# Kernel optimization log

Hardware: AMD Instinct MI355X
Metric: run time of the kernel (lower is better)

## Reference

```python
import jax, jax.numpy as jnp
import numpy as np

N = 100000   # nodes
E = 1600000  # edges (before self-loops)
IN = 128     # in_features
H = 4        # heads
C = 64       # out_features per head
D = H * C    # concat output dim = 256
NEG_SLOPE = 0.2
EPS = 1e-5


def setup_inputs() -> dict:
    key = jax.random.key(0)
    k = jax.random.split(key, 8)
    x = jax.random.normal(k[0], (N, IN), jnp.float32)
    edge_index = jax.random.randint(k[1], (2, E), 0, N, jnp.int32)
    # GATConv params (glorot-ish init)
    W = jax.random.normal(k[2], (IN, D), jnp.float32) * np.float32(np.sqrt(2.0 / (IN + D)))
    att_src = jax.random.normal(k[3], (H, C), jnp.float32) * np.float32(np.sqrt(2.0 / C))
    att_dst = jax.random.normal(k[4], (H, C), jnp.float32) * np.float32(np.sqrt(2.0 / C))
    bias = jnp.zeros((D,), jnp.float32)
    # LayerNorm params
    gamma = jnp.ones((D,), jnp.float32)
    beta = jnp.zeros((D,), jnp.float32)
    return {"x": x, "edge_index": edge_index, "W": W, "att_src": att_src,
            "att_dst": att_dst, "bias": bias, "gamma": gamma, "beta": beta}


def reference(x, edge_index, W, att_src, att_dst, bias, gamma, beta):
    # --- GATConv (add_self_loops=True, negative_slope=0.2, eval-mode dropout) ---
    loops = jnp.arange(N, dtype=edge_index.dtype)
    ei = jnp.concatenate([edge_index, jnp.stack([loops, loops])], axis=1)  # (2, E+N)
    src, dst = ei[0], ei[1]

    h = (x @ W).reshape(N, H, C)                       # (N,H,C)
    a_s = jnp.einsum('nhc,hc->nh', h, att_src)          # (N,H)
    a_d = jnp.einsum('nhc,hc->nh', h, att_dst)          # (N,H)

    logits = jax.nn.leaky_relu(a_s[src] + a_d[dst], NEG_SLOPE)  # (Etot,H)
    # segment softmax over incoming edges of each destination node
    mx = jax.ops.segment_max(logits, dst, num_segments=N)       # (N,H)
    ex = jnp.exp(logits - mx[dst])
    den = jax.ops.segment_sum(ex, dst, num_segments=N)          # (N,H)
    alpha = ex / den[dst]                                       # (Etot,H)

    msg = h[src] * alpha[:, :, None]                             # (Etot,H,C)
    out = jax.ops.segment_sum(msg, dst, num_segments=N)          # (N,H,C)
    out = out.reshape(N, D) + bias

    # --- ELU + LayerNorm (dropout = identity in eval) ---
    out = jax.nn.elu(out)
    mu = out.mean(-1, keepdims=True)
    var = out.var(-1, keepdims=True)
    out = (out - mu) * jax.lax.rsqrt(var + EPS) * gamma + beta
    return out
```

## Files before the change

### kernel.cpp

```cpp
#include <hip/hip_runtime.h>
#include <hip/hip_bf16.h>

#define IN_F 128
#define DF   256
#define HEADS 4
#define CPH  64
#define NEG  0.2f
#define LN_EPS 1e-5f

__device__ __forceinline__ float lrelu(float x) { return x > 0.f ? x : NEG * x; }
__device__ __forceinline__ float b2f(unsigned short u) {
    union { unsigned int i; float f; } v; v.i = ((unsigned int)u) << 16; return v.f;
}

__global__ __launch_bounds__(256) void k_gemm(
        const float* __restrict__ x, const float* __restrict__ W,
        const float* __restrict__ att_s, const float* __restrict__ att_d,
        __hip_bfloat16* __restrict__ hb,
        float* __restrict__ a_s, float* __restrict__ a_d, int N)
{
    __shared__ float xs[16 * IN_F];
    int t = threadIdx.x;
    int row0 = blockIdx.x * 16;

    const float4* xg = (const float4*)(x + (size_t)row0 * IN_F);
    float4* xs4 = (float4*)xs;
    #pragma unroll
    for (int j = 0; j < 2; ++j) {
        int s = t + j * 256;
        if (row0 + (s >> 5) < N) xs4[s] = xg[s];
        else xs4[s] = make_float4(0.f, 0.f, 0.f, 0.f);
    }
    __syncthreads();

    float acc[16];
    #pragma unroll
    for (int r = 0; r < 16; ++r) acc[r] = 0.f;

    const float* Wc = W + t;
    for (int k0 = 0; k0 < IN_F; k0 += 4) {
        float w0 = Wc[(k0 + 0) * DF];
        float w1 = Wc[(k0 + 1) * DF];
        float w2 = Wc[(k0 + 2) * DF];
        float w3 = Wc[(k0 + 3) * DF];
        #pragma unroll
        for (int r = 0; r < 16; ++r) {
            float4 xv = xs4[r * 32 + (k0 >> 2)];
            acc[r] = fmaf(xv.x, w0, fmaf(xv.y, w1, fmaf(xv.z, w2, fmaf(xv.w, w3, acc[r]))));
        }
    }

    int lane = t & 63, wid = t >> 6;
    float was = att_s[t], wad = att_d[t];
    #pragma unroll
    for (int r = 0; r < 16; ++r) {
        int row = row0 + r;
        if (row >= N) break;
        hb[(size_t)row * DF + t] = __float2bfloat16(acc[r]);
        float vs = acc[r] * was, vd = acc[r] * wad;
        #pragma unroll
        for (int m = 32; m >= 1; m >>= 1) {
            vs += __shfl_xor(vs, m, 64);
            vd += __shfl_xor(vd, m, 64);
        }
        if (lane == 0) { a_s[row * 4 + wid] = vs; a_d[row * 4 + wid] = vd; }
    }
}

__global__ void k_count(const int* __restrict__ dste, int E, int* __restrict__ indeg)
{
    for (int e = blockIdx.x * blockDim.x + threadIdx.x; e < E; e += gridDim.x * blockDim.x)
        atomicAdd(&indeg[dste[e]], 1);
}

__global__ __launch_bounds__(256) void k_scanA(const int* __restrict__ indeg, int N, int* __restrict__ part)
{
    int t = threadIdx.x, base = blockIdx.x * 1024;
    int s = 0;
    #pragma unroll
    for (int j = 0; j < 4; ++j) { int i = base + t * 4 + j; if (i < N) s += indeg[i]; }
    #pragma unroll
    for (int m = 32; m >= 1; m >>= 1) s += __shfl_xor(s, m, 64);
    __shared__ int red[4];
    if ((t & 63) == 0) red[t >> 6] = s;
    __syncthreads();
    if (t == 0) part[blockIdx.x] = red[0] + red[1] + red[2] + red[3];
}

__global__ __launch_bounds__(128) void k_scanB(const int* __restrict__ part, int NB, int* __restrict__ bloff)
{
    __shared__ int buf[128];
    int t = threadIdx.x;
    int v = (t < NB) ? part[t] : 0;
    buf[t] = v;
    __syncthreads();
    for (int off = 1; off < 128; off <<= 1) {
        int x2 = (t >= off) ? buf[t - off] : 0;
        __syncthreads();
        buf[t] += x2;
        __syncthreads();
    }
    if (t < NB) bloff[t] = buf[t] - v;
}

__global__ __launch_bounds__(256) void k_scanC(const int* __restrict__ indeg, int N,
        const int* __restrict__ bloff, int* __restrict__ offs, int* __restrict__ cur)
{
    int t = threadIdx.x, bid = blockIdx.x, base = bid * 1024;
    int v[4]; int s = 0;
    #pragma unroll
    for (int j = 0; j < 4; ++j) { int i = base + t * 4 + j; v[j] = (i < N) ? indeg[i] : 0; s += v[j]; }
    __shared__ int lds[256];
    lds[t] = s;
    __syncthreads();
    for (int off = 1; off < 256; off <<= 1) {
        int x2 = (t >= off) ? lds[t - off] : 0;
        __syncthreads();
        lds[t] += x2;
        __syncthreads();
    }
    int run = lds[t] - s + bloff[bid];
    #pragma unroll
    for (int j = 0; j < 4; ++j) {
        int i = base + t * 4 + j;
        if (i < N) { offs[i] = run; cur[i] = run; }
        run += v[j];
    }
    if (bid == (int)gridDim.x - 1 && t == 255) offs[N] = run;
}

__global__ void k_scatter(const int* __restrict__ srce, const int* __restrict__ dste, int E,
                          int* __restrict__ cur, int* __restrict__ srclist)
{
    for (int e = blockIdx.x * blockDim.x + threadIdx.x; e < E; e += gridDim.x * blockDim.x) {
        int d = dste[e];
        int p = atomicAdd(&cur[d], 1);
        srclist[p] = srce[e];
    }
}

__global__ __launch_bounds__(256) void k_gather(
        const __hip_bfloat16* __restrict__ hb,
        const float* __restrict__ a_s, const float* __restrict__ a_d,
        const int* __restrict__ offs, const int* __restrict__ srclist,
        const float* __restrict__ bias, const float* __restrict__ gamma,
        const float* __restrict__ beta, float* __restrict__ out, int N)
{
    int wid = threadIdx.x >> 6, lane = threadIdx.x & 63;
    int n = blockIdx.x * 4 + wid;
    if (n >= N) return;
    int head = lane >> 4;
    int d0 = lane << 2;

    float adh = a_d[(size_t)n * 4 + head];
    int beg = offs[n], end = offs[n + 1];

    float acc0, acc1, acc2, acc3, den;
    {
        float as = a_s[(size_t)n * 4 + head];
        float p = expf(lrelu(as + adh));
        den = p;
        ushort4 hv = *(const ushort4*)(hb + (size_t)n * DF + d0);
        acc0 = p * b2f(hv.x); acc1 = p * b2f(hv.y);
        acc2 = p * b2f(hv.z); acc3 = p * b2f(hv.w);
    }

    int e = beg;
    int s_next = (e < end) ? srclist[e] : 0;
    while (e < end) {
        int s = s_next;
        ++e;
        if (e < end) s_next = srclist[e];
        float as = a_s[(size_t)s * 4 + head];
        ushort4 hv = *(const ushort4*)(hb + (size_t)s * DF + d0);
        float p = expf(lrelu(as + adh));
        den += p;
        acc0 = fmaf(p, b2f(hv.x), acc0); acc1 = fmaf(p, b2f(hv.y), acc1);
        acc2 = fmaf(p, b2f(hv.z), acc2); acc3 = fmaf(p, b2f(hv.w), acc3);
    }

    float inv = 1.f / den;
    float4 bia = *(const float4*)(bias + d0);
    float v0 = fmaf(acc0, inv, bia.x);
    float v1 = fmaf(acc1, inv, bia.y);
    float v2 = fmaf(acc2, inv, bia.z);
    float v3 = fmaf(acc3, inv, bia.w);
    v0 = v0 > 0.f ? v0 : expm1f(v0);
    v1 = v1 > 0.f ? v1 : expm1f(v1);
    v2 = v2 > 0.f ? v2 : expm1f(v2);
    v3 = v3 > 0.f ? v3 : expm1f(v3);

    float s1 = v0 + v1 + v2 + v3;
    float s2 = v0 * v0 + v1 * v1 + v2 * v2 + v3 * v3;
    #pragma unroll
    for (int m = 32; m >= 1; m >>= 1) {
        s1 += __shfl_xor(s1, m, 64);
        s2 += __shfl_xor(s2, m, 64);
    }
    float mu = s1 * (1.f / 256.f);
    float var = s2 * (1.f / 256.f) - mu * mu;
    float rs = rsqrtf(var + LN_EPS);
    float4 g  = *(const float4*)(gamma + d0);
    float4 be = *(const float4*)(beta + d0);
    float4 o;
    o.x = (v0 - mu) * rs * g.x + be.x;
    o.y = (v1 - mu) * rs * g.y + be.y;
    o.z = (v2 - mu) * rs * g.z + be.z;
    o.w = (v3 - mu) * rs * g.w + be.w;
    *(float4*)(out + (size_t)n * DF + d0) = o;
}

extern "C" void kernel_launch(void* const* d_in, const int* in_sizes, int n_in,
                              void* d_out, int out_size, void* d_ws, size_t ws_size,
                              hipStream_t stream)
{
    const float* x     = (const float*)d_in[0];
    const int*   ei    = (const int*)d_in[1];
    const float* W     = (const float*)d_in[2];
    const float* att_s = (const float*)d_in[3];
    const float* att_d = (const float*)d_in[4];
    const float* bias  = (const float*)d_in[5];
    const float* gamma = (const float*)d_in[6];
    const float* beta  = (const float*)d_in[7];
    float* out = (float*)d_out;

    int N = in_sizes[0] / IN_F;
    int E = in_sizes[1] / 2;
    const int* srce = ei;
    const int* dste = ei + E;

    char* wsb = (char*)d_ws;
    size_t off = 0;
    auto alloc = [&](size_t bytes) -> void* {
        void* p = wsb + off;
        off += (bytes + 255) & ~(size_t)255;
        return p;
    };
    __hip_bfloat16* hb = (__hip_bfloat16*)alloc((size_t)N * DF * sizeof(__hip_bfloat16));
    float* a_s   = (float*)alloc((size_t)N * 4 * sizeof(float));
    float* a_d   = (float*)alloc((size_t)N * 4 * sizeof(float));
    int*   indeg = (int*)alloc((size_t)N * sizeof(int));
    int*   offs  = (int*)alloc(((size_t)N + 1) * sizeof(int));
    int*   cur   = (int*)alloc((size_t)N * sizeof(int));
    int*   srclist = (int*)alloc((size_t)E * sizeof(int));
    int NB = (N + 1023) / 1024;
    int* part  = (int*)alloc((size_t)NB * sizeof(int));
    int* bloff = (int*)alloc((size_t)NB * sizeof(int));

    hipMemsetAsync(indeg, 0, (size_t)N * sizeof(int), stream);

    k_gemm<<<(N + 15) / 16, 256, 0, stream>>>(x, W, att_s, att_d, hb, a_s, a_d, N);
    k_count<<<2048, 256, 0, stream>>>(dste, E, indeg);
    k_scanA<<<NB, 256, 0, stream>>>(indeg, N, part);
    k_scanB<<<1, 128, 0, stream>>>(part, NB, bloff);
    k_scanC<<<NB, 256, 0, stream>>>(indeg, N, bloff, offs, cur);
    k_scatter<<<2048, 256, 0, stream>>>(srce, dste, E, cur, srclist);
    k_gather<<<(N + 3) / 4, 256, 0, stream>>>(hb, a_s, a_d, offs, srclist, bias, gamma, beta, out, N);
}
```

Measured before the change: 639.5 us.

## Use bf16 MFMA for node projection GEMM and split attention-score kernel

Replaces the scalar fp32 FMA projection x@W with a bf16 MFMA 16x16x32 kernel. W is pre-packed into the MFMA B-fragment layout by a small pack kernel, and x is converted to bf16 into padded LDS. The per-head attention dot products move into a separate k_att kernel that reads the bf16 h back. This trades an extra pass over h and reduced input precision (x and W in bf16) for much higher GEMM throughput.

New measurement: 527.0 us. -17.6%, faster.

```diff
diff --git a/kernel.cpp b/kernel.cpp
--- a/kernel.cpp
+++ b/kernel.cpp
@@ -3,67 +3,130 @@
 
 #define IN_F 128
 #define DF   256
-#define HEADS 4
-#define CPH  64
 #define NEG  0.2f
 #define LN_EPS 1e-5f
+
+typedef __attribute__((ext_vector_type(8))) short bf16x8;
+typedef __attribute__((ext_vector_type(4))) float f32x4;
 
 __device__ __forceinline__ float lrelu(float x) { return x > 0.f ? x : NEG * x; }
 __device__ __forceinline__ float b2f(unsigned short u) {
     union { unsigned int i; float f; } v; v.i = ((unsigned int)u) << 16; return v.f;
 }
-
+__device__ __forceinline__ unsigned short f2b(float f) {
+    union { float f; unsigned int i; } v; v.f = f;
+    unsigned int r = v.i + 0x7FFFu + ((v.i >> 16) & 1u);
+    return (unsigned short)(r >> 16);
+}
+
+__global__ __launch_bounds__(256) void k_pack(const float* __restrict__ W,
+                                              unsigned short* __restrict__ Wp)
+{
+    int t = blockIdx.x * 256 + threadIdx.x;
+    if (t >= 16 * 4 * 64) return;
+    int lane = t & 63, ks = (t >> 6) & 3, ct = t >> 8;
+    int col = ct * 16 + (lane & 15);
+    int kb  = ks * 32 + (lane >> 4) * 8;
+    unsigned short* dst = Wp + (size_t)t * 8;
+    #pragma unroll
+    for (int j = 0; j < 8; ++j)
+        dst[j] = f2b(W[(size_t)(kb + j) * DF + col]);
+}
+
+#define APAD 136
 __global__ __launch_bounds__(256) void k_gemm(
-        const float* __restrict__ x, const float* __restrict__ W,
+        const float* __restrict__ x, const unsigned short* __restrict__ Wp,
+        unsigned short* __restrict__ hb, int N)
+{
+    __shared__ unsigned short lds_a[64 * APAD];
+    int t = threadIdx.x;
+    int row0 = blockIdx.x * 64;
+
+    const float4* xg = (const float4*)x;
+    #pragma unroll
+    for (int j = 0; j < 8; ++j) {
+        int s = t + j * 256;
+        int r = s >> 5, c4 = s & 31;
+        ushort4 w = make_ushort4(0, 0, 0, 0);
+        if (row0 + r < N) {
+            float4 xv = xg[(size_t)(row0 + r) * 32 + c4];
+            w = make_ushort4(f2b(xv.x), f2b(xv.y), f2b(xv.z), f2b(xv.w));
+        }
+        *(ushort4*)(&lds_a[r * APAD + c4 * 4]) = w;
+    }
+    __syncthreads();
+
+    int lane = t & 63, wid = t >> 6;
+    int rbase = (wid & 1) * 32;
+    int cbase = (wid >> 1) * 128;
+    int ct0 = cbase >> 4;
+
+    bf16x8 af[2][4];
+    #pragma unroll
+    for (int rt = 0; rt < 2; ++rt)
+        #pragma unroll
+        for (int ks = 0; ks < 4; ++ks) {
+            int r = rbase + rt * 16 + (lane & 15);
+            int k = ks * 32 + (lane >> 4) * 8;
+            af[rt][ks] = *(const bf16x8*)(&lds_a[r * APAD + k]);
+        }
+
+    f32x4 acc[2][8];
+    #pragma unroll
+    for (int rt = 0; rt < 2; ++rt)
+        #pragma unroll
+        for (int ct = 0; ct < 8; ++ct)
+            acc[rt][ct] = (f32x4){0.f, 0.f, 0.f, 0.f};
+
+    const bf16x8* Wp8 = (const bf16x8*)Wp;
+    #pragma unroll
+    for (int ct = 0; ct < 8; ++ct) {
+        #pragma unroll
+        for (int ks = 0; ks < 4; ++ks) {
+            bf16x8 b = Wp8[((ct0 + ct) * 4 + ks) * 64 + lane];
+            acc[0][ct] = __builtin_amdgcn_mfma_f32_16x16x32_bf16(af[0][ks], b, acc[0][ct], 0, 0, 0);
+            acc[1][ct] = __builtin_amdgcn_mfma_f32_16x16x32_bf16(af[1][ks], b, acc[1][ct], 0, 0, 0);
+        }
+    }
+
+    #pragma unroll
+    for (int rt = 0; rt < 2; ++rt) {
+        #pragma unroll
+        for (int ct = 0; ct < 8; ++ct) {
+            int col = cbase + ct * 16 + (lane & 15);
+            #pragma unroll
+            for (int r = 0; r < 4; ++r) {
+                int row = row0 + rbase + rt * 16 + (lane >> 4) * 4 + r;
+                if (row < N)
+                    hb[(size_t)row * DF + col] = f2b(acc[rt][ct][r]);
+            }
+        }
+    }
+}
+
+__global__ __launch_bounds__(256) void k_att(
+        const unsigned short* __restrict__ hb,
         const float* __restrict__ att_s, const float* __restrict__ att_d,
-        __hip_bfloat16* __restrict__ hb,
         float* __restrict__ a_s, float* __restrict__ a_d, int N)
 {
-    __shared__ float xs[16 * IN_F];
-    int t = threadIdx.x;
-    int row0 = blockIdx.x * 16;
-
-    const float4* xg = (const float4*)(x + (size_t)row0 * IN_F);
-    float4* xs4 = (float4*)xs;
-    #pragma unroll
-    for (int j = 0; j < 2; ++j) {
-        int s = t + j * 256;
-        if (row0 + (s >> 5) < N) xs4[s] = xg[s];
-        else xs4[s] = make_float4(0.f, 0.f, 0.f, 0.f);
-    }
-    __syncthreads();
-
-    float acc[16];
-    #pragma unroll
-    for (int r = 0; r < 16; ++r) acc[r] = 0.f;
-
-    const float* Wc = W + t;
-    for (int k0 = 0; k0 < IN_F; k0 += 4) {
-        float w0 = Wc[(k0 + 0) * DF];
-        float w1 = Wc[(k0 + 1) * DF];
-        float w2 = Wc[(k0 + 2) * DF];
-        float w3 = Wc[(k0 + 3) * DF];
-        #pragma unroll
-        for (int r = 0; r < 16; ++r) {
-            float4 xv = xs4[r * 32 + (k0 >> 2)];
-            acc[r] = fmaf(xv.x, w0, fmaf(xv.y, w1, fmaf(xv.z, w2, fmaf(xv.w, w3, acc[r]))));
-        }
-    }
-
-    int lane = t & 63, wid = t >> 6;
-    float was = att_s[t], wad = att_d[t];
-    #pragma unroll
-    for (int r = 0; r < 16; ++r) {
-        int row = row0 + r;
-        if (row >= N) break;
-        hb[(size_t)row * DF + t] = __float2bfloat16(acc[r]);
-        float vs = acc[r] * was, vd = acc[r] * wad;
-        #pragma unroll
-        for (int m = 32; m >= 1; m >>= 1) {
-            vs += __shfl_xor(vs, m, 64);
-            vd += __shfl_xor(vd, m, 64);
-        }
-        if (lane == 0) { a_s[row * 4 + wid] = vs; a_d[row * 4 + wid] = vd; }
+    int wid = threadIdx.x >> 6, lane = threadIdx.x & 63;
+    int n = blockIdx.x * 4 + wid;
+    if (n >= N) return;
+    int d0 = lane << 2, head = lane >> 4;
+    ushort4 hv = *(const ushort4*)(hb + (size_t)n * DF + d0);
+    float4 as4 = *(const float4*)(att_s + d0);
+    float4 ad4 = *(const float4*)(att_d + d0);
+    float h0 = b2f(hv.x), h1 = b2f(hv.y), h2 = b2f(hv.z), h3 = b2f(hv.w);
+    float vs = h0 * as4.x + h1 * as4.y + h2 * as4.z + h3 * as4.w;
+    float vd = h0 * ad4.x + h1 * ad4.y + h2 * ad4.z + h3 * ad4.w;
+    #pragma unroll
+    for (int m = 8; m >= 1; m >>= 1) {
+        vs += __shfl_xor(vs, m, 64);
+        vd += __shfl_xor(vd, m, 64);
+    }
+    if ((lane & 15) == 0) {
+        a_s[(size_t)n * 4 + head] = vs;
+        a_d[(size_t)n * 4 + head] = vd;
     }
 }
 
@@ -140,7 +203,7 @@
 }
 
 __global__ __launch_bounds__(256) void k_gather(
-        const __hip_bfloat16* __restrict__ hb,
+        const unsigned short* __restrict__ hb,
         const float* __restrict__ a_s, const float* __restrict__ a_d,
         const int* __restrict__ offs, const int* __restrict__ srclist,
         const float* __restrict__ bias, const float* __restrict__ gamma,
@@ -236,7 +299,8 @@
         off += (bytes + 255) & ~(size_t)255;
         return p;
     };
-    __hip_bfloat16* hb = (__hip_bfloat16*)alloc((size_t)N * DF * sizeof(__hip_bfloat16));
+    unsigned short* hb = (unsigned short*)alloc((size_t)N * DF * sizeof(unsigned short));
+    unsigned short* Wp = (unsigned short*)alloc((size_t)IN_F * DF * sizeof(unsigned short));
     float* a_s   = (float*)alloc((size_t)N * 4 * sizeof(float));
     float* a_d   = (float*)alloc((size_t)N * 4 * sizeof(float));
     int*   indeg = (int*)alloc((size_t)N * sizeof(int));
@@ -247,9 +311,11 @@
     int* part  = (int*)alloc((size_t)NB * sizeof(int));
     int* bloff = (int*)alloc((size_t)NB * sizeof(int));
 
-    hipMemsetAsync(indeg, 0, (size_t)N * sizeof(int), stream);
-
-    k_gemm<<<(N + 15) / 16, 256, 0, stream>>>(x, W, att_s, att_d, hb, a_s, a_d, N);
+    (void)hipMemsetAsync(indeg, 0, (size_t)N * sizeof(int), stream);
+
+    k_pack<<<16, 256, 0, stream>>>(W, Wp);
+    k_gemm<<<(N + 63) / 64, 256, 0, stream>>>(x, Wp, hb, N);
+    k_att<<<(N + 3) / 4, 256, 0, stream>>>(hb, att_s, att_d, a_s, a_d, N);
     k_count<<<2048, 256, 0, stream>>>(dste, E, indeg);
     k_scanA<<<NB, 256, 0, stream>>>(indeg, N, part);
     k_scanB<<<1, 128, 0, stream>>>(part, NB, bloff);
```
